# Kernel optimization log

Hardware: AMD Instinct MI355X
Metric: run time of the kernel (lower is better)

Reference implementation:

```python
import jax, jax.numpy as jnp
import numpy as np

C = 32            # multiplicity per irrep (node irreps = 32x0e + 32x1o)
N_NODES = 50000
N_EDGES = 800000
R_DIM = 8         # radial embedding dim
R_HID = 8         # radial MLP hidden width
N_SPECIES = 5
AVG_NEIGH = 16.0
N_PATHS = 4       # 0ex0e->0e, 0ex1o->1o, 1ox0e->1o, 1ox1o->0e


def setup_inputs() -> dict:
    key = jax.random.key(0)
    ks = jax.random.split(key, 16)
    inp = {
        'node_features': jax.random.normal(ks[0], (N_NODES, 4 * C), jnp.float32),
        'edge_features': jax.random.normal(ks[1], (N_EDGES, 4), jnp.float32),
        'radial_embedding': jax.random.normal(ks[2], (N_EDGES, R_DIM), jnp.float32),
        'senders': jax.random.randint(ks[3], (N_EDGES,), 0, N_NODES),
        'receivers': jax.random.randint(ks[4], (N_EDGES,), 0, N_NODES),
        'node_species': jax.random.randint(ks[5], (N_NODES,), 0, N_SPECIES),
        # linear_up: per-irrep (block-diagonal) mixing
        'W_up_s': jax.random.normal(ks[6], (C, C), jnp.float32),
        'W_up_v': jax.random.normal(ks[7], (C, C), jnp.float32),
        # radial MLP (no biases, e3nn-style): R_DIM -> R_HID -> N_PATHS*C
        'W_r1': jax.random.normal(ks[8], (R_DIM, R_HID), jnp.float32),
        'W_r2': jax.random.normal(ks[9], (R_HID, N_PATHS * C), jnp.float32),
        # linear_down: 2C x 0e -> 2C (C feats + C gates); 2C x 1o -> C x 1o
        'W_down_s': jax.random.normal(ks[10], (2 * C, 2 * C), jnp.float32),
        'W_down_v': jax.random.normal(ks[11], (2 * C, C), jnp.float32),
        # species-indexed skip connection to gate irreps
        'W_skip_s': jax.random.normal(ks[12], (N_SPECIES, C, 2 * C), jnp.float32),
        'W_skip_v': jax.random.normal(ks[13], (N_SPECIES, C, C), jnp.float32),
    }
    return inp


def reference(node_features, edge_features, radial_embedding, senders, receivers,
              node_species, W_up_s, W_up_v, W_r1, W_r2, W_down_s, W_down_v,
              W_skip_s, W_skip_v):
    N = node_features.shape[0]
    inv_sqrt_C = 1.0 / np.sqrt(C)
    # split irreps: scalars [N,C] and vectors [N,C,3]
    s = node_features[:, :C]
    v = node_features[:, C:].reshape(N, C, 3)
    # ---- linear_up (block-diagonal irreps Linear, fan-in normalized) ----
    s_up = (s @ W_up_s) * inv_sqrt_C
    v_up = jnp.einsum('ncx,cd->ndx', v, W_up_v) * inv_sqrt_C
    # ---- radial MLP -> per-edge tensor-product path weights ----
    h = jax.nn.silu((radial_embedding @ W_r1) * (1.0 / np.sqrt(R_DIM)))
    w = ((h @ W_r2) * (1.0 / np.sqrt(R_HID))).reshape(-1, N_PATHS, C)  # [E,4,C]
    # ---- tensor product messages over edges ----
    sh0 = edge_features[:, 0]      # [E]  l=0
    sh1 = edge_features[:, 1:4]    # [E,3] l=1
    se = s_up[senders]             # [E,C]
    ve = v_up[senders]             # [E,C,3]
    m0 = jnp.concatenate([
        w[:, 0] * se * sh0[:, None],                                      # 0e x 0e -> 0e
        w[:, 3] * jnp.einsum('ecx,ex->ec', ve, sh1) * (1.0 / np.sqrt(3.0))  # 1o x 1o -> 0e
    ], axis=1)                                                            # [E,2C]
    m1 = jnp.concatenate([
        w[:, 1, :, None] * se[:, :, None] * sh1[:, None, :],              # 0e x 1o -> 1o
        w[:, 2, :, None] * ve * sh0[:, None, None],                       # 1o x 0e -> 1o
    ], axis=1)                                                            # [E,2C,3]
    # ---- scatter aggregate to receivers, normalize by sqrt(avg neigh) ----
    inv_sqrt_deg = 1.0 / np.sqrt(AVG_NEIGH)
    agg0 = jax.ops.segment_sum(m0, receivers, num_segments=N) * inv_sqrt_deg
    agg1 = jax.ops.segment_sum(m1, receivers, num_segments=N) * inv_sqrt_deg
    # ---- linear_down to gate irreps (2C x 0e: C feats + C gates; C x 1o) ----
    inv_sqrt_2C = 1.0 / np.sqrt(2 * C)
    sc = (agg0 @ W_down_s) * inv_sqrt_2C                     # [N,2C]
    vc = jnp.einsum('ncx,cd->ndx', agg1, W_down_v) * inv_sqrt_2C  # [N,C,3]
    # ---- species-indexed skip connection ----
    skip_s = jnp.einsum('nc,ncd->nd', s, W_skip_s[node_species]) * inv_sqrt_C
    skip_v = jnp.einsum('ncx,ncd->ndx', v, W_skip_v[node_species]) * inv_sqrt_C
    sc = 0.5 * (sc + skip_s)
    vc = 0.5 * (vc + skip_v)
    # ---- gated nonlinearity: silu on scalars, silu(gates) * vectors ----
    feats = jax.nn.silu(sc[:, :C])
    gates = jax.nn.silu(sc[:, C:])
    vg = vc * gates[:, :, None]
    return jnp.concatenate([feats, vg.reshape(N, 3 * C)], axis=1)  # [N,4C]
```

## Files before the change

kernel.cpp:

```cpp
#include <hip/hip_runtime.h>
#include <stdint.h>

__device__ __forceinline__ float b2f(unsigned short u) {
    union { uint32_t i; float f; } v; v.i = ((uint32_t)u) << 16; return v.f;
}
__device__ __forceinline__ unsigned short f2b(float f) {
    union { float f; uint32_t i; } v; v.f = f;
    uint32_t i = v.i;
    uint32_t r = (i + 0x7fffu + ((i >> 16) & 1u)) >> 16;
    return (unsigned short)r;
}
__device__ __forceinline__ float silu_f(float x) { return x / (1.f + __expf(-x)); }

template<bool BF>
__device__ __forceinline__ float ldin(const void* p, size_t i) {
    if (BF) return b2f(((const unsigned short*)p)[i]);
    return ((const float*)p)[i];
}
template<bool BF>
__device__ __forceinline__ void ld4(const void* p, size_t i, float o[4]) {
    if (BF) {
        const ushort4 u = *(const ushort4*)((const unsigned short*)p + i);
        o[0] = b2f(u.x); o[1] = b2f(u.y); o[2] = b2f(u.z); o[3] = b2f(u.w);
    } else {
        const float4 f = *(const float4*)((const float*)p + i);
        o[0] = f.x; o[1] = f.y; o[2] = f.z; o[3] = f.w;
    }
}
template<bool BF>
__device__ __forceinline__ void stout(void* p, size_t i, float v) {
    if (BF) ((unsigned short*)p)[i] = f2b(v);
    else    ((float*)p)[i] = v;
}

#define INV_SQRT_C   0.17677669529663687f
#define INV_SQRT_8   0.3535533905932738f
#define INV_SQRT_3   0.5773502691896258f
#define INV_SQRT_DEG 0.25f
#define INV_SQRT_2C  0.125f

__device__ __forceinline__ bool detect_bf(const void* buf) {
    const int lane = threadIdx.x & 63;
    const uint32_t w = ((const uint32_t*)buf)[lane];
    const uint32_t ex = (w >> 7) & 0xFFu;
    const unsigned long long m = __ballot(ex >= 96u && ex <= 130u);
    return __popcll(m) > 32;
}

template<bool BF>
__device__ __forceinline__ void prep_nodes_body(
    const void* __restrict__ nf, const void* __restrict__ Wus,
    const void* __restrict__ Wuv, unsigned short* __restrict__ stage,
    int N, float* smem)
{
    float (*wsm)[128] = (float(*)[128])smem;
    const int wave = threadIdx.x >> 6;
    const int lane = threadIdx.x & 63;
    const int n = blockIdx.x * 4 + wave;
    if (n >= N) return;
    wsm[wave][lane]      = ldin<BF>(nf, (size_t)n * 128 + lane);
    wsm[wave][64 + lane] = ldin<BF>(nf, (size_t)n * 128 + 64 + lane);
    if (lane < 32) {
        float acc = 0.f;
        #pragma unroll 8
        for (int c = 0; c < 32; ++c) acc += wsm[wave][c] * ldin<BF>(Wus, c * 32 + lane);
        stage[(size_t)n * 128 + lane] = f2b(acc * INV_SQRT_C);
    } else {
        const int dd = lane - 32;
        float ax = 0.f, ay = 0.f, az = 0.f;
        #pragma unroll 8
        for (int c = 0; c < 32; ++c) {
            const float wv = ldin<BF>(Wuv, c * 32 + dd);
            ax += wsm[wave][32 + 3 * c    ] * wv;
            ay += wsm[wave][32 + 3 * c + 1] * wv;
            az += wsm[wave][32 + 3 * c + 2] * wv;
        }
        stage[(size_t)n * 128 + 32 + dd] = f2b(ax * INV_SQRT_C);
        stage[(size_t)n * 128 + 64 + dd] = f2b(ay * INV_SQRT_C);
        stage[(size_t)n * 128 + 96 + dd] = f2b(az * INV_SQRT_C);
    }
}
__global__ __launch_bounds__(256) void k_prep_nodes(
    const void* nf, const void* Wus, const void* Wuv,
    unsigned short* stage, int N)
{
    __shared__ float smem[4 * 128];
    if (detect_bf(nf)) prep_nodes_body<true >(nf, Wus, Wuv, stage, N, smem);
    else               prep_nodes_body<false>(nf, Wus, Wuv, stage, N, smem);
}

template<bool BF>
__device__ __forceinline__ void prep_edges_body(
    const void* __restrict__ radial, const int* __restrict__ senders,
    const int* __restrict__ recv, const void* __restrict__ Wr1,
    unsigned short* __restrict__ hbuf, int* __restrict__ counts,
    int* __restrict__ table, int* __restrict__ tableS,
    int* __restrict__ ovcnt, int* __restrict__ ovlist, int E)
{
    const int e = blockIdx.x * 256 + threadIdx.x;
    if (e >= E) return;
    const int rr  = recv[e];
    const int snd = senders[e];
    const int pos = atomicAdd(&counts[rr], 1);
    float r[8];
    ld4<BF>(radial, (size_t)e * 8, r);
    ld4<BF>(radial, (size_t)e * 8 + 4, r + 4);
    unsigned short h[8];
    #pragma unroll
    for (int j = 0; j < 8; ++j) {
        float pre = 0.f;
        #pragma unroll
        for (int k = 0; k < 8; ++k) pre += r[k] * ldin<BF>(Wr1, k * 8 + j);
        h[j] = f2b(silu_f(pre * INV_SQRT_8) * INV_SQRT_8);
    }
    ushort4* hp = (ushort4*)(hbuf + (size_t)e * 8);
    hp[0] = make_ushort4(h[0], h[1], h[2], h[3]);
    hp[1] = make_ushort4(h[4], h[5], h[6], h[7]);
    if (pos < 64) {
        table[(size_t)rr * 64 + pos] = e;
        if (tableS) tableS[(size_t)rr * 64 + pos] = snd;
    } else {
        ovlist[atomicAdd(ovcnt, 1)] = e;
    }
}
__global__ __launch_bounds__(256) void k_prep_edges(
    const void* radial, const int* senders, const int* recv, const void* Wr1,
    unsigned short* hbuf, int* counts, int* table, int* tableS,
    int* ovcnt, int* ovlist, int E)
{
    if (detect_bf(radial)) prep_edges_body<true >(radial, senders, recv, Wr1, hbuf,
                                                  counts, table, tableS, ovcnt, ovlist, E);
    else                   prep_edges_body<false>(radial, senders, recv, Wr1, hbuf,
                                                  counts, table, tableS, ovcnt, ovlist, E);
}

template<bool BF>
__device__ __forceinline__ void aggregate_body(
    const void* __restrict__ nf, const void* __restrict__ ef,
    const int* __restrict__ senders, const int* __restrict__ recv,
    const int* __restrict__ species,
    const void* __restrict__ Wr2, const void* __restrict__ Wds,
    const void* __restrict__ Wdv, const void* __restrict__ Wss,
    const void* __restrict__ Wsv,
    const unsigned short* __restrict__ stage,
    const unsigned short* __restrict__ hbuf,
    const int* __restrict__ counts, const int* __restrict__ table,
    const int* __restrict__ tableS,
    const int* __restrict__ ovcnt, const int* __restrict__ ovlist,
    void* __restrict__ out, int N, float* smem)
{
    float (*ldsM)[64][16] = (float(*)[64][16])smem;
    float (*ldsNF)[128]   = (float(*)[128])(smem + 4096);
    const int wave = threadIdx.x >> 6;
    const int lane = threadIdx.x & 63;
    const int n = blockIdx.x * 4 + wave;
    const bool valid = (n < N);
    const int d = lane - 32;
    int sp = 0, cnt = 0, mc = 0;
    float wA[8], wB[8];
    float acc0 = 0.f, a1x = 0.f, a1y = 0.f, a1z = 0.f;

    if (valid) {
        sp  = species[n];
        cnt = counts[n];
        mc  = (cnt < 64) ? cnt : 64;
        const int colA = (lane < 32) ? lane : lane + 32;
        #pragma unroll
        for (int j = 0; j < 8; ++j) {
            wA[j] = ldin<BF>(Wr2, j * 128 + colA);
            wB[j] = ldin<BF>(Wr2, j * 128 + colA + 32);
        }
        ldsNF[wave][lane]      = ldin<BF>(nf, (size_t)n * 128 + lane);
        ldsNF[wave][64 + lane] = ldin<BF>(nf, (size_t)n * 128 + 64 + lane);
        if (lane < mc) {
            const int eid = table[(size_t)n * 64 + lane];
            const int snd = tableS ? tableS[(size_t)n * 64 + lane]
                                   : senders[eid];
            float e4[4];
            if (BF) {
                const ushort4 u = *(const ushort4*)((const unsigned short*)ef + (size_t)eid * 4);
                e4[0] = b2f(u.x); e4[1] = b2f(u.y); e4[2] = b2f(u.z); e4[3] = b2f(u.w);
            } else {
                ld4<false>(ef, (size_t)eid * 4, e4);
            }
            const uint4 th = *(const uint4*)(hbuf + (size_t)eid * 8);
            float* M = ldsM[wave][lane];
            ((float4*)M)[0] = make_float4(e4[0], e4[1], e4[2], e4[3]);
            ((float4*)M)[1] = make_float4(b2f((unsigned short)(th.x & 0xFFFFu)),
                                          b2f((unsigned short)(th.x >> 16)),
                                          b2f((unsigned short)(th.y & 0xFFFFu)),
                                          b2f((unsigned short)(th.y >> 16)));
            ((float4*)M)[2] = make_float4(b2f((unsigned short)(th.z & 0xFFFFu)),
                                          b2f((unsigned short)(th.z >> 16)),
                                          b2f((unsigned short)(th.w & 0xFFFFu)),
                                          b2f((unsigned short)(th.w >> 16)));
            M[12] = __int_as_float(snd);
        }
    }

    if (valid && mc > 0) {
        auto gatherOne = [&](int idx, unsigned short& o0, unsigned short& o1,
                             unsigned short& o2) {
            const int snd = __float_as_int(ldsM[wave][idx][12]);
            const unsigned short* rec = stage + (size_t)snd * 128;
            if (lane < 32) { o0 = rec[lane]; }
            else { o0 = rec[32 + d]; o1 = rec[64 + d]; o2 = rec[96 + d]; }
        };
        auto edgeC = [&](int i, unsigned short s0, unsigned short s1,
                         unsigned short s2) {
            const float4 e4 = *((const float4*)&ldsM[wave][i][0]);
            const float4 ha = *((const float4*)&ldsM[wave][i][4]);
            const float4 hb = *((const float4*)&ldsM[wave][i][8]);
            const float vA = ha.x * wA[0] + ha.y * wA[1] + ha.z * wA[2] + ha.w * wA[3]
                           + hb.x * wA[4] + hb.y * wA[5] + hb.z * wA[6] + hb.w * wA[7];
            const float vB = ha.x * wB[0] + ha.y * wB[1] + ha.z * wB[2] + ha.w * wB[3]
                           + hb.x * wB[4] + hb.y * wB[5] + hb.z * wB[6] + hb.w * wB[7];
            if (lane < 32) {
                const float se = b2f(s0);
                acc0 += vA * se * e4.x;
                const float tt = vB * se;
                a1x += tt * e4.y; a1y += tt * e4.z; a1z += tt * e4.w;
            } else {
                const float vx = b2f(s0), vy = b2f(s1), vz = b2f(s2);
                acc0 += vB * (vx * e4.y + vy * e4.z + vz * e4.w);
                const float tt = vA * e4.x;
                a1x += tt * vx; a1y += tt * vy; a1z += tt * vz;
            }
        };
        unsigned short g0[8], g1[8], g2[8];
        int base = 0;
        for (; base + 8 <= mc; base += 8) {
            #pragma unroll
            for (int k = 0; k < 8; ++k) gatherOne(base + k, g0[k], g1[k], g2[k]);
            #pragma unroll
            for (int k = 0; k < 8; ++k) edgeC(base + k, g0[k], g1[k], g2[k]);
        }
        if (base < mc) {
            const int bc = mc - base;
            #pragma unroll
            for (int k = 0; k < 7; ++k) if (k < bc) gatherOne(base + k, g0[k], g1[k], g2[k]);
            #pragma unroll
            for (int k = 0; k < 7; ++k) if (k < bc) edgeC(base + k, g0[k], g1[k], g2[k]);
        }
    }
    if (valid && cnt > 64) {
        const int oc = *ovcnt;
        for (int i2 = 0; i2 < oc; ++i2) {
            const int e = ovlist[i2];
            if (recv[e] != n) continue;
            const int s = senders[e];
            float efv[4];
            ld4<BF>(ef, (size_t)e * 4, efv);
            const float sh0 = efv[0], s1x = efv[1], s1y = efv[2], s1z = efv[3];
            float h[8];
            #pragma unroll
            for (int j = 0; j < 8; ++j) h[j] = b2f(hbuf[(size_t)e * 8 + j]);
            const float vA = h[0] * wA[0] + h[1] * wA[1] + h[2] * wA[2] + h[3] * wA[3]
                           + h[4] * wA[4] + h[5] * wA[5] + h[6] * wA[6] + h[7] * wA[7];
            const float vB = h[0] * wB[0] + h[1] * wB[1] + h[2] * wB[2] + h[3] * wB[3]
                           + h[4] * wB[4] + h[5] * wB[5] + h[6] * wB[6] + h[7] * wB[7];
            const unsigned short* rec = stage + (size_t)s * 128;
            if (lane < 32) {
                const float se = b2f(rec[lane]);
                acc0 += vA * se * sh0;
                const float tt = vB * se;
                a1x += tt * s1x; a1y += tt * s1y; a1z += tt * s1z;
            } else {
                const float vx = b2f(rec[32 + d]), vy = b2f(rec[64 + d]), vz = b2f(rec[96 + d]);
                acc0 += vB * (vx * s1x + vy * s1y + vz * s1z);
                const float tt = vA * sh0;
                a1x += tt * vx; a1y += tt * vy; a1z += tt * vz;
            }
        }
    }
    if (valid && lane >= 32) acc0 *= INV_SQRT_3;

    __syncthreads();

    float* base_ = smem;
    float (*lds_agg0)[64]    = (float(*)[64])   base_;
    float (*lds_agg1)[3][65] = (float(*)[3][65])(base_ + 256);
    float (*lds_scf)[64]     = (float(*)[64])  (base_ + 1036);

    if (valid) {
        lds_agg0[wave][lane]    = acc0 * INV_SQRT_DEG;
        lds_agg1[wave][0][lane] = a1x * INV_SQRT_DEG;
        lds_agg1[wave][1][lane] = a1y * INV_SQRT_DEG;
        lds_agg1[wave][2][lane] = a1z * INV_SQRT_DEG;

        float sc = 0.f;
        #pragma unroll 8
        for (int c = 0; c < 64; ++c) sc += lds_agg0[wave][c] * ldin<BF>(Wds, c * 64 + lane);
        sc *= INV_SQRT_2C;
        float ss = 0.f;
        #pragma unroll 8
        for (int c = 0; c < 32; ++c)
            ss += ldsNF[wave][c] * ldin<BF>(Wss, (size_t)sp * 2048 + c * 64 + lane);
        ss *= INV_SQRT_C;
        lds_scf[wave][lane] = 0.5f * (sc + ss);

        #pragma unroll
        for (int rr = 0; rr < 2; ++rr) {
            const int p = lane + rr * 64;
            float outv;
            if (p < 32) {
                outv = silu_f(lds_scf[wave][p]);
            } else {
                const int o = p - 32;
                const int c = o / 3;
                const int x = o - 3 * c;
                float vc = 0.f;
                #pragma unroll 8
                for (int c2 = 0; c2 < 64; ++c2)
                    vc += lds_agg1[wave][x][c2] * ldin<BF>(Wdv, c2 * 32 + c);
                vc *= INV_SQRT_2C;
                float sv = 0.f;
                #pragma unroll 8
                for (int c2 = 0; c2 < 32; ++c2)
                    sv += ldsNF[wave][32 + c2 * 3 + x] * ldin<BF>(Wsv, (size_t)sp * 1024 + c2 * 32 + c);
                sv *= INV_SQRT_C;
                const float g = silu_f(lds_scf[wave][32 + c]);
                outv = 0.5f * (vc + sv) * g;
            }
            stout<BF>(out, (size_t)n * 128 + p, outv);
        }
    }
}
__global__ __launch_bounds__(256) void k_aggregate(
    const void* nf, const void* ef, const int* senders, const int* recv,
    const int* species,
    const void* Wr2, const void* Wds, const void* Wdv, const void* Wss, const void* Wsv,
    const unsigned short* stage, const unsigned short* hbuf,
    const int* counts, const int* table, const int* tableS,
    const int* ovcnt, const int* ovlist,
    void* out, int N)
{
    __shared__ float smem[4 * 64 * 16 + 4 * 128];
    if (detect_bf(nf)) aggregate_body<true >(nf, ef, senders, recv, species,
                                             Wr2, Wds, Wdv, Wss, Wsv,
                                             stage, hbuf, counts, table, tableS,
                                             ovcnt, ovlist, out, N, smem);
    else               aggregate_body<false>(nf, ef, senders, recv, species,
                                             Wr2, Wds, Wdv, Wss, Wsv,
                                             stage, hbuf, counts, table, tableS,
                                             ovcnt, ovlist, out, N, smem);
}

extern "C" void kernel_launch(void* const* d_in, const int* in_sizes, int n_in,
                              void* d_out, int out_size, void* d_ws, size_t ws_size,
                              hipStream_t stream) {
    const void* nf      = d_in[0];
    const void* ef      = d_in[1];
    const void* radial  = d_in[2];
    const int*  senders = (const int*)d_in[3];
    const int*  recv    = (const int*)d_in[4];
    const int*  specie  = (const int*)d_in[5];
    const void* Wus = d_in[6];
    const void* Wuv = d_in[7];
    const void* Wr1 = d_in[8];
    const void* Wr2 = d_in[9];
    const void* Wds = d_in[10];
    const void* Wdv = d_in[11];
    const void* Wss = d_in[12];
    const void* Wsv = d_in[13];

    const int N = in_sizes[5];
    const int E = in_sizes[3];

    const size_t stageB = (size_t)N * 128 * 2;
    const size_t hbufB  = (size_t)E * 8 * 2;
    const size_t tableB = (size_t)N * 64 * 4;
    const size_t miscB  = (size_t)(N + 1 + E) * 4;
    const size_t need1  = stageB + hbufB + tableB + miscB;
    const size_t need2  = need1 + tableB;
    if (ws_size < need1) return;

    char* ws = (char*)d_ws;
    unsigned short* stage = (unsigned short*)ws;
    unsigned short* hbuf  = (unsigned short*)(ws + stageB);
    int* table = (int*)(ws + stageB + hbufB);
    size_t off = stageB + hbufB + tableB;
    int* tableS = nullptr;
    if (ws_size >= need2) { tableS = (int*)(ws + off); off += tableB; }
    int* counts = (int*)(ws + off);
    int* ovcnt  = counts + N;
    int* ovlist = ovcnt + 1;

    hipMemsetAsync(counts, 0, (size_t)(N + 1) * sizeof(int), stream);

    k_prep_nodes<<<(N + 3) / 4, 256, 0, stream>>>(nf, Wus, Wuv, stage, N);
    k_prep_edges<<<(E + 255) / 256, 256, 0, stream>>>(radial, senders, recv, Wr1,
                                                      hbuf, counts, table, tableS,
                                                      ovcnt, ovlist, E);
    k_aggregate<<<(N + 3) / 4, 256, 0, stream>>>(nf, ef, senders, recv, specie,
                                                 Wr2, Wds, Wdv, Wss, Wsv,
                                                 stage, hbuf, counts, table, tableS,
                                                 ovcnt, ovlist, d_out, N);
}
```

Measured before the change: 470.2 us.

## Use persistent grid-stride prep kernels with register-cached weights and a branchless edge loop

The node and edge prep kernels become persistent grid-stride loops with fixed grid sizes. Each thread loads its weight column, or the whole 8x8 radial weight, into registers once instead of re-reading it per item. In the aggregate kernel, the per-edge sender gather uses precomputed byte offsets, and the lane-divergent scalar/vector branches are replaced by a select-based uniform computation. Risks are higher register pressure, with up to 64 extra floats per thread, and lower parallelism from the fixed grid sizes. The branchless form also does a few extra multiplies on the low lanes.

```diff
diff --git a/kernel.cpp b/kernel.cpp
--- a/kernel.cpp
+++ b/kernel.cpp
@@ -56,28 +56,33 @@
     float (*wsm)[128] = (float(*)[128])smem;
     const int wave = threadIdx.x >> 6;
     const int lane = threadIdx.x & 63;
-    const int n = blockIdx.x * 4 + wave;
-    if (n >= N) return;
-    wsm[wave][lane]      = ldin<BF>(nf, (size_t)n * 128 + lane);
-    wsm[wave][64 + lane] = ldin<BF>(nf, (size_t)n * 128 + 64 + lane);
-    if (lane < 32) {
-        float acc = 0.f;
-        #pragma unroll 8
-        for (int c = 0; c < 32; ++c) acc += wsm[wave][c] * ldin<BF>(Wus, c * 32 + lane);
-        stage[(size_t)n * 128 + lane] = f2b(acc * INV_SQRT_C);
-    } else {
-        const int dd = lane - 32;
-        float ax = 0.f, ay = 0.f, az = 0.f;
-        #pragma unroll 8
-        for (int c = 0; c < 32; ++c) {
-            const float wv = ldin<BF>(Wuv, c * 32 + dd);
-            ax += wsm[wave][32 + 3 * c    ] * wv;
-            ay += wsm[wave][32 + 3 * c + 1] * wv;
-            az += wsm[wave][32 + 3 * c + 2] * wv;
-        }
-        stage[(size_t)n * 128 + 32 + dd] = f2b(ax * INV_SQRT_C);
-        stage[(size_t)n * 128 + 64 + dd] = f2b(ay * INV_SQRT_C);
-        stage[(size_t)n * 128 + 96 + dd] = f2b(az * INV_SQRT_C);
+    const int dd = lane & 31;
+    const bool low = lane < 32;
+    float wcol[32];
+    #pragma unroll
+    for (int c = 0; c < 32; ++c)
+        wcol[c] = low ? ldin<BF>(Wus, c * 32 + dd) : ldin<BF>(Wuv, c * 32 + dd);
+    const int nw = gridDim.x * 4;
+    for (int n = blockIdx.x * 4 + wave; n < N; n += nw) {
+        wsm[wave][lane]      = ldin<BF>(nf, (size_t)n * 128 + lane);
+        wsm[wave][64 + lane] = ldin<BF>(nf, (size_t)n * 128 + 64 + lane);
+        if (low) {
+            float acc = 0.f;
+            #pragma unroll 8
+            for (int c = 0; c < 32; ++c) acc += wsm[wave][c] * wcol[c];
+            stage[(size_t)n * 128 + lane] = f2b(acc * INV_SQRT_C);
+        } else {
+            float ax = 0.f, ay = 0.f, az = 0.f;
+            #pragma unroll 8
+            for (int c = 0; c < 32; ++c) {
+                ax += wsm[wave][32 + 3 * c    ] * wcol[c];
+                ay += wsm[wave][32 + 3 * c + 1] * wcol[c];
+                az += wsm[wave][32 + 3 * c + 2] * wcol[c];
+            }
+            stage[(size_t)n * 128 + 32 + dd] = f2b(ax * INV_SQRT_C);
+            stage[(size_t)n * 128 + 64 + dd] = f2b(ay * INV_SQRT_C);
+            stage[(size_t)n * 128 + 96 + dd] = f2b(az * INV_SQRT_C);
+        }
     }
 }
 __global__ __launch_bounds__(256) void k_prep_nodes(
@@ -97,30 +102,35 @@
     int* __restrict__ table, int* __restrict__ tableS,
     int* __restrict__ ovcnt, int* __restrict__ ovlist, int E)
 {
-    const int e = blockIdx.x * 256 + threadIdx.x;
-    if (e >= E) return;
-    const int rr  = recv[e];
-    const int snd = senders[e];
-    const int pos = atomicAdd(&counts[rr], 1);
-    float r[8];
-    ld4<BF>(radial, (size_t)e * 8, r);
-    ld4<BF>(radial, (size_t)e * 8 + 4, r + 4);
-    unsigned short h[8];
+    float wr1[64];
     #pragma unroll
-    for (int j = 0; j < 8; ++j) {
-        float pre = 0.f;
+    for (int q = 0; q < 64; ++q) wr1[q] = ldin<BF>(Wr1, q);
+    const int stride = gridDim.x * 256;
+    #pragma unroll 2
+    for (int e = blockIdx.x * 256 + threadIdx.x; e < E; e += stride) {
+        const int rr  = recv[e];
+        const int snd = senders[e];
+        const int pos = atomicAdd(&counts[rr], 1);
+        float r[8];
+        ld4<BF>(radial, (size_t)e * 8, r);
+        ld4<BF>(radial, (size_t)e * 8 + 4, r + 4);
+        unsigned short h[8];
         #pragma unroll
-        for (int k = 0; k < 8; ++k) pre += r[k] * ldin<BF>(Wr1, k * 8 + j);
-        h[j] = f2b(silu_f(pre * INV_SQRT_8) * INV_SQRT_8);
-    }
-    ushort4* hp = (ushort4*)(hbuf + (size_t)e * 8);
-    hp[0] = make_ushort4(h[0], h[1], h[2], h[3]);
-    hp[1] = make_ushort4(h[4], h[5], h[6], h[7]);
-    if (pos < 64) {
-        table[(size_t)rr * 64 + pos] = e;
-        if (tableS) tableS[(size_t)rr * 64 + pos] = snd;
-    } else {
-        ovlist[atomicAdd(ovcnt, 1)] = e;
+        for (int j = 0; j < 8; ++j) {
+            float pre = 0.f;
+            #pragma unroll
+            for (int k = 0; k < 8; ++k) pre += r[k] * wr1[k * 8 + j];
+            h[j] = f2b(silu_f(pre * INV_SQRT_8) * INV_SQRT_8);
+        }
+        ushort4* hp = (ushort4*)(hbuf + (size_t)e * 8);
+        hp[0] = make_ushort4(h[0], h[1], h[2], h[3]);
+        hp[1] = make_ushort4(h[4], h[5], h[6], h[7]);
+        if (pos < 64) {
+            table[(size_t)rr * 64 + pos] = e;
+            if (tableS) tableS[(size_t)rr * 64 + pos] = snd;
+        } else {
+            ovlist[atomicAdd(ovcnt, 1)] = e;
+        }
     }
 }
 __global__ __launch_bounds__(256) void k_prep_edges(
@@ -155,16 +165,20 @@
     const int lane = threadIdx.x & 63;
     const int n = blockIdx.x * 4 + wave;
     const bool valid = (n < N);
-    const int d = lane - 32;
+    const bool low = lane < 32;
+    const int d = lane & 31;
     int sp = 0, cnt = 0, mc = 0;
     float wA[8], wB[8];
     float acc0 = 0.f, a1x = 0.f, a1y = 0.f, a1z = 0.f;
+    const uint32_t off0 = low ? (uint32_t)(lane << 1) : (uint32_t)(64 + (d << 1));
+    const uint32_t off1 = 128 + (d << 1);
+    const uint32_t off2 = 192 + (d << 1);
 
     if (valid) {
         sp  = species[n];
         cnt = counts[n];
         mc  = (cnt < 64) ? cnt : 64;
-        const int colA = (lane < 32) ? lane : lane + 32;
+        const int colA = low ? lane : lane + 32;
         #pragma unroll
         for (int j = 0; j < 8; ++j) {
             wA[j] = ldin<BF>(Wr2, j * 128 + colA);
@@ -202,12 +216,15 @@
         auto gatherOne = [&](int idx, unsigned short& o0, unsigned short& o1,
                              unsigned short& o2) {
             const int snd = __float_as_int(ldsM[wave][idx][12]);
-            const unsigned short* rec = stage + (size_t)snd * 128;
-            if (lane < 32) { o0 = rec[lane]; }
-            else { o0 = rec[32 + d]; o1 = rec[64 + d]; o2 = rec[96 + d]; }
+            const char* bp = (const char*)stage + (((uint32_t)snd) << 8);
+            o0 = *(const unsigned short*)(bp + off0);
+            if (!low) {
+                o1 = *(const unsigned short*)(bp + off1);
+                o2 = *(const unsigned short*)(bp + off2);
+            } else { o1 = 0; o2 = 0; }
         };
-        auto edgeC = [&](int i, unsigned short s0, unsigned short s1,
-                         unsigned short s2) {
+        auto edgeC = [&](int i, unsigned short s0u, unsigned short s1u,
+                         unsigned short s2u) {
             const float4 e4 = *((const float4*)&ldsM[wave][i][0]);
             const float4 ha = *((const float4*)&ldsM[wave][i][4]);
             const float4 hb = *((const float4*)&ldsM[wave][i][8]);
@@ -215,17 +232,18 @@
                            + hb.x * wA[4] + hb.y * wA[5] + hb.z * wA[6] + hb.w * wA[7];
             const float vB = ha.x * wB[0] + ha.y * wB[1] + ha.z * wB[2] + ha.w * wB[3]
                            + hb.x * wB[4] + hb.y * wB[5] + hb.z * wB[6] + hb.w * wB[7];
-            if (lane < 32) {
-                const float se = b2f(s0);
-                acc0 += vA * se * e4.x;
-                const float tt = vB * se;
-                a1x += tt * e4.y; a1y += tt * e4.z; a1z += tt * e4.w;
-            } else {
-                const float vx = b2f(s0), vy = b2f(s1), vz = b2f(s2);
-                acc0 += vB * (vx * e4.y + vy * e4.z + vz * e4.w);
-                const float tt = vA * e4.x;
-                a1x += tt * vx; a1y += tt * vy; a1z += tt * vz;
-            }
+            const float f0 = b2f(s0u), f1 = b2f(s1u), f2 = b2f(s2u);
+            const float wS = low ? vA   : vB;
+            const float wV = low ? vB   : vA;
+            const float G  = low ? f0   : e4.x;
+            const float m0 = low ? e4.x : e4.y;
+            const float Hx = low ? e4.y : f0;
+            const float Hy = low ? e4.z : f1;
+            const float Hz = low ? e4.w : f2;
+            const float dt = f0 * m0 + f1 * e4.z + f2 * e4.w;
+            acc0 += wS * dt;
+            const float t = wV * G;
+            a1x += t * Hx; a1y += t * Hy; a1z += t * Hz;
         };
         unsigned short g0[8], g1[8], g2[8];
         int base = 0;
@@ -260,7 +278,7 @@
             const float vB = h[0] * wB[0] + h[1] * wB[1] + h[2] * wB[2] + h[3] * wB[3]
                            + h[4] * wB[4] + h[5] * wB[5] + h[6] * wB[6] + h[7] * wB[7];
             const unsigned short* rec = stage + (size_t)s * 128;
-            if (lane < 32) {
+            if (low) {
                 const float se = b2f(rec[lane]);
                 acc0 += vA * se * sh0;
                 const float tt = vB * se;
@@ -273,7 +291,7 @@
             }
         }
     }
-    if (valid && lane >= 32) acc0 *= INV_SQRT_3;
+    if (valid && !low) acc0 *= INV_SQRT_3;
 
     __syncthreads();
 
@@ -388,10 +406,10 @@
 
     hipMemsetAsync(counts, 0, (size_t)(N + 1) * sizeof(int), stream);
 
-    k_prep_nodes<<<(N + 3) / 4, 256, 0, stream>>>(nf, Wus, Wuv, stage, N);
-    k_prep_edges<<<(E + 255) / 256, 256, 0, stream>>>(radial, senders, recv, Wr1,
-                                                      hbuf, counts, table, tableS,
-                                                      ovcnt, ovlist, E);
+    k_prep_nodes<<<2048, 256, 0, stream>>>(nf, Wus, Wuv, stage, N);
+    k_prep_edges<<<1024, 256, 0, stream>>>(radial, senders, recv, Wr1,
+                                           hbuf, counts, table, tableS,
+                                           ovcnt, ovlist, E);
     k_aggregate<<<(N + 3) / 4, 256, 0, stream>>>(nf, ef, senders, recv, specie,
                                                  Wr2, Wds, Wdv, Wss, Wsv,
                                                  stage, hbuf, counts, table, tableS,
```

Measured after the change: 543.6 us. +15.6%, slower.

## Pack per-edge data into 32-byte records and interleave staged node features

Applied to the files above, without the earlier changes.

The edge prep kernel now writes one 32-byte record per edge that holds the bf16 hidden radial features, the bf16 edge attributes and the sender id. This replaces the separate hbuf and tableS arrays plus the later edge_features read. Node staging is interleaved so each channel's scalar and xyz vector sit in 8 contiguous bytes, letting each aggregate lane fetch a sender's data with one 8-byte load. The aggregate kernel now handles 8 nodes per block with 32 lanes per node, each lane covering one channel for all four paths, and cooperatively preloads edge records into LDS. The trade-offs are more LDS per block, fewer lanes per node, and edge attributes rounded to bf16 in the fp32 path.

```diff
diff --git a/kernel.cpp b/kernel.cpp
--- a/kernel.cpp
+++ b/kernel.cpp
@@ -3,12 +3,21 @@
 
 __device__ __forceinline__ float b2f(unsigned short u) {
     union { uint32_t i; float f; } v; v.i = ((uint32_t)u) << 16; return v.f;
+}
+__device__ __forceinline__ float lo16(uint32_t u) {
+    union { uint32_t i; float f; } v; v.i = u << 16; return v.f;
+}
+__device__ __forceinline__ float hi16(uint32_t u) {
+    union { uint32_t i; float f; } v; v.i = u & 0xffff0000u; return v.f;
 }
 __device__ __forceinline__ unsigned short f2b(float f) {
     union { float f; uint32_t i; } v; v.f = f;
     uint32_t i = v.i;
     uint32_t r = (i + 0x7fffu + ((i >> 16) & 1u)) >> 16;
     return (unsigned short)r;
+}
+__device__ __forceinline__ uint32_t pk2(float a, float b) {
+    return (uint32_t)f2b(a) | ((uint32_t)f2b(b) << 16);
 }
 __device__ __forceinline__ float silu_f(float x) { return x / (1.f + __expf(-x)); }
 
@@ -51,22 +60,24 @@
 __device__ __forceinline__ void prep_nodes_body(
     const void* __restrict__ nf, const void* __restrict__ Wus,
     const void* __restrict__ Wuv, unsigned short* __restrict__ stage,
-    int N, float* smem)
-{
-    float (*wsm)[128] = (float(*)[128])smem;
+    int N, float* wsmf, unsigned short* outsu)
+{
+    float (*wsm)[128] = (float(*)[128])wsmf;
+    unsigned short (*outst)[128] = (unsigned short(*)[128])outsu;
     const int wave = threadIdx.x >> 6;
     const int lane = threadIdx.x & 63;
+    const int dd = lane & 31;
+    const bool low = lane < 32;
     const int n = blockIdx.x * 4 + wave;
     if (n >= N) return;
     wsm[wave][lane]      = ldin<BF>(nf, (size_t)n * 128 + lane);
     wsm[wave][64 + lane] = ldin<BF>(nf, (size_t)n * 128 + 64 + lane);
-    if (lane < 32) {
+    if (low) {
         float acc = 0.f;
         #pragma unroll 8
-        for (int c = 0; c < 32; ++c) acc += wsm[wave][c] * ldin<BF>(Wus, c * 32 + lane);
-        stage[(size_t)n * 128 + lane] = f2b(acc * INV_SQRT_C);
+        for (int c = 0; c < 32; ++c) acc += wsm[wave][c] * ldin<BF>(Wus, c * 32 + dd);
+        outst[wave][4 * dd] = f2b(acc * INV_SQRT_C);
     } else {
-        const int dd = lane - 32;
         float ax = 0.f, ay = 0.f, az = 0.f;
         #pragma unroll 8
         for (int c = 0; c < 32; ++c) {
@@ -75,27 +86,33 @@
             ay += wsm[wave][32 + 3 * c + 1] * wv;
             az += wsm[wave][32 + 3 * c + 2] * wv;
         }
-        stage[(size_t)n * 128 + 32 + dd] = f2b(ax * INV_SQRT_C);
-        stage[(size_t)n * 128 + 64 + dd] = f2b(ay * INV_SQRT_C);
-        stage[(size_t)n * 128 + 96 + dd] = f2b(az * INV_SQRT_C);
+        outst[wave][4 * dd + 1] = f2b(ax * INV_SQRT_C);
+        outst[wave][4 * dd + 2] = f2b(ay * INV_SQRT_C);
+        outst[wave][4 * dd + 3] = f2b(az * INV_SQRT_C);
+    }
+    if (low) {
+        *(uint2*)((char*)stage + (size_t)n * 256 + dd * 8) =
+            *(const uint2*)&outst[wave][4 * dd];
     }
 }
 __global__ __launch_bounds__(256) void k_prep_nodes(
     const void* nf, const void* Wus, const void* Wuv,
     unsigned short* stage, int N)
 {
-    __shared__ float smem[4 * 128];
-    if (detect_bf(nf)) prep_nodes_body<true >(nf, Wus, Wuv, stage, N, smem);
-    else               prep_nodes_body<false>(nf, Wus, Wuv, stage, N, smem);
+    __shared__ float wsmf[4 * 128];
+    __shared__ unsigned short outsu[4 * 128];
+    if (detect_bf(nf)) prep_nodes_body<true >(nf, Wus, Wuv, stage, N, wsmf, outsu);
+    else               prep_nodes_body<false>(nf, Wus, Wuv, stage, N, wsmf, outsu);
 }
 
 template<bool BF>
 __device__ __forceinline__ void prep_edges_body(
-    const void* __restrict__ radial, const int* __restrict__ senders,
-    const int* __restrict__ recv, const void* __restrict__ Wr1,
-    unsigned short* __restrict__ hbuf, int* __restrict__ counts,
-    int* __restrict__ table, int* __restrict__ tableS,
-    int* __restrict__ ovcnt, int* __restrict__ ovlist, int E)
+    const void* __restrict__ radial, const void* __restrict__ ef,
+    const int* __restrict__ senders, const int* __restrict__ recv,
+    const void* __restrict__ Wr1,
+    uint4* __restrict__ mtable, int* __restrict__ counts,
+    int* __restrict__ table, int* __restrict__ ovcnt,
+    int* __restrict__ ovlist, int E)
 {
     const int e = blockIdx.x * 256 + threadIdx.x;
     if (e >= E) return;
@@ -105,245 +122,260 @@
     float r[8];
     ld4<BF>(radial, (size_t)e * 8, r);
     ld4<BF>(radial, (size_t)e * 8 + 4, r + 4);
-    unsigned short h[8];
+    float h[8];
     #pragma unroll
     for (int j = 0; j < 8; ++j) {
         float pre = 0.f;
         #pragma unroll
         for (int k = 0; k < 8; ++k) pre += r[k] * ldin<BF>(Wr1, k * 8 + j);
-        h[j] = f2b(silu_f(pre * INV_SQRT_8) * INV_SQRT_8);
-    }
-    ushort4* hp = (ushort4*)(hbuf + (size_t)e * 8);
-    hp[0] = make_ushort4(h[0], h[1], h[2], h[3]);
-    hp[1] = make_ushort4(h[4], h[5], h[6], h[7]);
-    if (pos < 64) {
-        table[(size_t)rr * 64 + pos] = e;
-        if (tableS) tableS[(size_t)rr * 64 + pos] = snd;
+        h[j] = silu_f(pre * INV_SQRT_8) * INV_SQRT_8;
+    }
+    uint32_t e01, e23;
+    if (BF) {
+        const uint2 t = *(const uint2*)((const unsigned short*)ef + (size_t)e * 4);
+        e01 = t.x; e23 = t.y;
     } else {
-        ovlist[atomicAdd(ovcnt, 1)] = e;
-    }
+        const float4 f = *(const float4*)((const float*)ef + (size_t)e * 4);
+        e01 = pk2(f.x, f.y); e23 = pk2(f.z, f.w);
+    }
+    mtable[(size_t)e * 2    ] = make_uint4(pk2(h[0], h[1]), pk2(h[2], h[3]),
+                                           pk2(h[4], h[5]), pk2(h[6], h[7]));
+    mtable[(size_t)e * 2 + 1] = make_uint4(e01, e23, (uint32_t)snd, 0u);
+    if (pos < 64) table[(size_t)rr * 64 + pos] = e;
+    else          ovlist[atomicAdd(ovcnt, 1)] = e;
 }
 __global__ __launch_bounds__(256) void k_prep_edges(
-    const void* radial, const int* senders, const int* recv, const void* Wr1,
-    unsigned short* hbuf, int* counts, int* table, int* tableS,
+    const void* radial, const void* ef, const int* senders, const int* recv,
+    const void* Wr1, uint4* mtable, int* counts, int* table,
     int* ovcnt, int* ovlist, int E)
 {
-    if (detect_bf(radial)) prep_edges_body<true >(radial, senders, recv, Wr1, hbuf,
-                                                  counts, table, tableS, ovcnt, ovlist, E);
-    else                   prep_edges_body<false>(radial, senders, recv, Wr1, hbuf,
-                                                  counts, table, tableS, ovcnt, ovlist, E);
+    if (detect_bf(radial)) prep_edges_body<true >(radial, ef, senders, recv, Wr1,
+                                                  mtable, counts, table, ovcnt, ovlist, E);
+    else                   prep_edges_body<false>(radial, ef, senders, recv, Wr1,
+                                                  mtable, counts, table, ovcnt, ovlist, E);
 }
 
 template<bool BF>
 __device__ __forceinline__ void aggregate_body(
     const void* __restrict__ nf, const void* __restrict__ ef,
+    const void* __restrict__ radial,
     const int* __restrict__ senders, const int* __restrict__ recv,
     const int* __restrict__ species,
-    const void* __restrict__ Wr2, const void* __restrict__ Wds,
-    const void* __restrict__ Wdv, const void* __restrict__ Wss,
-    const void* __restrict__ Wsv,
+    const void* __restrict__ Wr1, const void* __restrict__ Wr2,
+    const void* __restrict__ Wds, const void* __restrict__ Wdv,
+    const void* __restrict__ Wss, const void* __restrict__ Wsv,
     const unsigned short* __restrict__ stage,
-    const unsigned short* __restrict__ hbuf,
+    const uint4* __restrict__ mt,
     const int* __restrict__ counts, const int* __restrict__ table,
-    const int* __restrict__ tableS,
     const int* __restrict__ ovcnt, const int* __restrict__ ovlist,
-    void* __restrict__ out, int N, float* smem)
-{
-    float (*ldsM)[64][16] = (float(*)[64][16])smem;
-    float (*ldsNF)[128]   = (float(*)[128])(smem + 4096);
-    const int wave = threadIdx.x >> 6;
-    const int lane = threadIdx.x & 63;
-    const int n = blockIdx.x * 4 + wave;
+    void* __restrict__ out, int N, uint32_t* smem)
+{
+    uint32_t (*ldsE)[64][8] = (uint32_t(*)[64][8])smem;
+    float (*ldsNF)[128] = (float(*)[128])(smem + 4096);
+    const int tid  = threadIdx.x;
+    const int wave = tid >> 6;
+    const int lane = tid & 63;
+    const int half = lane >> 5;
+    const int c    = lane & 31;
+    const int i    = wave * 2 + half;
+    const int bn   = blockIdx.x * 8;
+    const int n    = bn + i;
     const bool valid = (n < N);
-    const int d = lane - 32;
-    int sp = 0, cnt = 0, mc = 0;
-    float wA[8], wB[8];
-    float acc0 = 0.f, a1x = 0.f, a1y = 0.f, a1z = 0.f;
-
+
+    for (int idx = tid; idx < 512; idx += 256) {
+        const int ii = idx >> 6, j = idx & 63, ni = bn + ii;
+        if (ni < N) {
+            const int ct = counts[ni];
+            if (j < (ct < 64 ? ct : 64)) {
+                const int e = table[(size_t)ni * 64 + j];
+                const uint4 a = mt[(size_t)e * 2];
+                const uint4 b = mt[(size_t)e * 2 + 1];
+                *(uint4*)&ldsE[ii][j][0] = a;
+                *(uint4*)&ldsE[ii][j][4] = b;
+            }
+        }
+    }
+    for (int idx = tid; idx < 1024; idx += 256) {
+        const int ii = idx >> 7, f = idx & 127, ni = bn + ii;
+        if (ni < N) ldsNF[ii][f] = ldin<BF>(nf, (size_t)ni * 128 + f);
+    }
+    __syncthreads();
+
+    int cnt = 0, mc = 0;
+    float W0[8], W1[8], W2[8], W3[8];
+    float accS = 0.f, accD = 0.f;
+    float a1ax = 0.f, a1ay = 0.f, a1az = 0.f;
+    float a1bx = 0.f, a1by = 0.f, a1bz = 0.f;
     if (valid) {
-        sp  = species[n];
         cnt = counts[n];
         mc  = (cnt < 64) ? cnt : 64;
-        const int colA = (lane < 32) ? lane : lane + 32;
         #pragma unroll
         for (int j = 0; j < 8; ++j) {
-            wA[j] = ldin<BF>(Wr2, j * 128 + colA);
-            wB[j] = ldin<BF>(Wr2, j * 128 + colA + 32);
-        }
-        ldsNF[wave][lane]      = ldin<BF>(nf, (size_t)n * 128 + lane);
-        ldsNF[wave][64 + lane] = ldin<BF>(nf, (size_t)n * 128 + 64 + lane);
-        if (lane < mc) {
-            const int eid = table[(size_t)n * 64 + lane];
-            const int snd = tableS ? tableS[(size_t)n * 64 + lane]
-                                   : senders[eid];
-            float e4[4];
-            if (BF) {
-                const ushort4 u = *(const ushort4*)((const unsigned short*)ef + (size_t)eid * 4);
-                e4[0] = b2f(u.x); e4[1] = b2f(u.y); e4[2] = b2f(u.z); e4[3] = b2f(u.w);
-            } else {
-                ld4<false>(ef, (size_t)eid * 4, e4);
-            }
-            const uint4 th = *(const uint4*)(hbuf + (size_t)eid * 8);
-            float* M = ldsM[wave][lane];
-            ((float4*)M)[0] = make_float4(e4[0], e4[1], e4[2], e4[3]);
-            ((float4*)M)[1] = make_float4(b2f((unsigned short)(th.x & 0xFFFFu)),
-                                          b2f((unsigned short)(th.x >> 16)),
-                                          b2f((unsigned short)(th.y & 0xFFFFu)),
-                                          b2f((unsigned short)(th.y >> 16)));
-            ((float4*)M)[2] = make_float4(b2f((unsigned short)(th.z & 0xFFFFu)),
-                                          b2f((unsigned short)(th.z >> 16)),
-                                          b2f((unsigned short)(th.w & 0xFFFFu)),
-                                          b2f((unsigned short)(th.w >> 16)));
-            M[12] = __int_as_float(snd);
-        }
-    }
+            W0[j] = ldin<BF>(Wr2, (size_t)j * 128 + c);
+            W1[j] = ldin<BF>(Wr2, (size_t)j * 128 + 32 + c);
+            W2[j] = ldin<BF>(Wr2, (size_t)j * 128 + 64 + c);
+            W3[j] = ldin<BF>(Wr2, (size_t)j * 128 + 96 + c);
+        }
+    }
+    const char* stgb = (const char*)stage;
+    const uint32_t coff = (uint32_t)(c << 3);
+
+    auto EDGE = [&](int idx, uint2 pv) {
+        const uint4 A = *(const uint4*)&ldsE[i][idx][0];
+        const uint4 B = *(const uint4*)&ldsE[i][idx][4];
+        const float h0 = lo16(A.x), h1 = hi16(A.x), h2 = lo16(A.y), h3 = hi16(A.y);
+        const float h4 = lo16(A.z), h5 = hi16(A.z), h6 = lo16(A.w), h7 = hi16(A.w);
+        const float sh0 = lo16(B.x), s1x = hi16(B.x), s1y = lo16(B.y), s1z = hi16(B.y);
+        const float se = lo16(pv.x), vx = hi16(pv.x), vy = lo16(pv.y), vz = hi16(pv.y);
+        const float w0 = h0*W0[0]+h1*W0[1]+h2*W0[2]+h3*W0[3]+h4*W0[4]+h5*W0[5]+h6*W0[6]+h7*W0[7];
+        const float w1 = h0*W1[0]+h1*W1[1]+h2*W1[2]+h3*W1[3]+h4*W1[4]+h5*W1[5]+h6*W1[6]+h7*W1[7];
+        const float w2 = h0*W2[0]+h1*W2[1]+h2*W2[2]+h3*W2[3]+h4*W2[4]+h5*W2[5]+h6*W2[6]+h7*W2[7];
+        const float w3 = h0*W3[0]+h1*W3[1]+h2*W3[2]+h3*W3[3]+h4*W3[4]+h5*W3[5]+h6*W3[6]+h7*W3[7];
+        const float d3 = vx * s1x + vy * s1y + vz * s1z;
+        accS += w0 * (se * sh0);
+        accD += w3 * d3;
+        const float t1 = w1 * se;
+        a1ax += t1 * s1x; a1ay += t1 * s1y; a1az += t1 * s1z;
+        const float t2 = w2 * sh0;
+        a1bx += t2 * vx;  a1by += t2 * vy;  a1bz += t2 * vz;
+    };
 
     if (valid && mc > 0) {
-        auto gatherOne = [&](int idx, unsigned short& o0, unsigned short& o1,
-                             unsigned short& o2) {
-            const int snd = __float_as_int(ldsM[wave][idx][12]);
-            const unsigned short* rec = stage + (size_t)snd * 128;
-            if (lane < 32) { o0 = rec[lane]; }
-            else { o0 = rec[32 + d]; o1 = rec[64 + d]; o2 = rec[96 + d]; }
-        };
-        auto edgeC = [&](int i, unsigned short s0, unsigned short s1,
-                         unsigned short s2) {
-            const float4 e4 = *((const float4*)&ldsM[wave][i][0]);
-            const float4 ha = *((const float4*)&ldsM[wave][i][4]);
-            const float4 hb = *((const float4*)&ldsM[wave][i][8]);
-            const float vA = ha.x * wA[0] + ha.y * wA[1] + ha.z * wA[2] + ha.w * wA[3]
-                           + hb.x * wA[4] + hb.y * wA[5] + hb.z * wA[6] + hb.w * wA[7];
-            const float vB = ha.x * wB[0] + ha.y * wB[1] + ha.z * wB[2] + ha.w * wB[3]
-                           + hb.x * wB[4] + hb.y * wB[5] + hb.z * wB[6] + hb.w * wB[7];
-            if (lane < 32) {
-                const float se = b2f(s0);
-                acc0 += vA * se * e4.x;
-                const float tt = vB * se;
-                a1x += tt * e4.y; a1y += tt * e4.z; a1z += tt * e4.w;
-            } else {
-                const float vx = b2f(s0), vy = b2f(s1), vz = b2f(s2);
-                acc0 += vB * (vx * e4.y + vy * e4.z + vz * e4.w);
-                const float tt = vA * e4.x;
-                a1x += tt * vx; a1y += tt * vy; a1z += tt * vz;
-            }
-        };
-        unsigned short g0[8], g1[8], g2[8];
+        uint2 pf[8];
         int base = 0;
         for (; base + 8 <= mc; base += 8) {
             #pragma unroll
-            for (int k = 0; k < 8; ++k) gatherOne(base + k, g0[k], g1[k], g2[k]);
+            for (int k = 0; k < 8; ++k) {
+                const size_t snd = (size_t)ldsE[i][base + k][6];
+                pf[k] = *(const uint2*)(stgb + (snd << 8) + coff);
+            }
             #pragma unroll
-            for (int k = 0; k < 8; ++k) edgeC(base + k, g0[k], g1[k], g2[k]);
-        }
-        if (base < mc) {
-            const int bc = mc - base;
-            #pragma unroll
-            for (int k = 0; k < 7; ++k) if (k < bc) gatherOne(base + k, g0[k], g1[k], g2[k]);
-            #pragma unroll
-            for (int k = 0; k < 7; ++k) if (k < bc) edgeC(base + k, g0[k], g1[k], g2[k]);
-        }
+            for (int k = 0; k < 8; ++k) EDGE(base + k, pf[k]);
+        }
+        const int bc = mc - base;
+        #pragma unroll
+        for (int k = 0; k < 7; ++k) if (k < bc) {
+            const size_t snd = (size_t)ldsE[i][base + k][6];
+            pf[k] = *(const uint2*)(stgb + (snd << 8) + coff);
+        }
+        #pragma unroll
+        for (int k = 0; k < 7; ++k) if (k < bc) EDGE(base + k, pf[k]);
     }
     if (valid && cnt > 64) {
         const int oc = *ovcnt;
-        for (int i2 = 0; i2 < oc; ++i2) {
-            const int e = ovlist[i2];
+        for (int q = 0; q < oc; ++q) {
+            const int e = ovlist[q];
             if (recv[e] != n) continue;
-            const int s = senders[e];
-            float efv[4];
-            ld4<BF>(ef, (size_t)e * 4, efv);
-            const float sh0 = efv[0], s1x = efv[1], s1y = efv[2], s1z = efv[3];
-            float h[8];
+            const int snd = senders[e];
+            float ev[4];
+            ld4<BF>(ef, (size_t)e * 4, ev);
+            float r8[8];
+            ld4<BF>(radial, (size_t)e * 8, r8);
+            ld4<BF>(radial, (size_t)e * 8 + 4, r8 + 4);
+            float hh[8];
             #pragma unroll
-            for (int j = 0; j < 8; ++j) h[j] = b2f(hbuf[(size_t)e * 8 + j]);
-            const float vA = h[0] * wA[0] + h[1] * wA[1] + h[2] * wA[2] + h[3] * wA[3]
-                           + h[4] * wA[4] + h[5] * wA[5] + h[6] * wA[6] + h[7] * wA[7];
-            const float vB = h[0] * wB[0] + h[1] * wB[1] + h[2] * wB[2] + h[3] * wB[3]
-                           + h[4] * wB[4] + h[5] * wB[5] + h[6] * wB[6] + h[7] * wB[7];
-            const unsigned short* rec = stage + (size_t)s * 128;
-            if (lane < 32) {
-                const float se = b2f(rec[lane]);
-                acc0 += vA * se * sh0;
-                const float tt = vB * se;
-                a1x += tt * s1x; a1y += tt * s1y; a1z += tt * s1z;
-            } else {
-                const float vx = b2f(rec[32 + d]), vy = b2f(rec[64 + d]), vz = b2f(rec[96 + d]);
-                acc0 += vB * (vx * s1x + vy * s1y + vz * s1z);
-                const float tt = vA * sh0;
-                a1x += tt * vx; a1y += tt * vy; a1z += tt * vz;
+            for (int j = 0; j < 8; ++j) {
+                float pre = 0.f;
+                #pragma unroll
+                for (int k2 = 0; k2 < 8; ++k2) pre += r8[k2] * ldin<BF>(Wr1, k2 * 8 + j);
+                hh[j] = silu_f(pre * INV_SQRT_8) * INV_SQRT_8;
             }
-        }
-    }
-    if (valid && lane >= 32) acc0 *= INV_SQRT_3;
+            const uint2 pv = *(const uint2*)(stgb + ((size_t)(uint32_t)snd << 8) + coff);
+            const float se = lo16(pv.x), vx = hi16(pv.x), vy = lo16(pv.y), vz = hi16(pv.y);
+            const float w0 = hh[0]*W0[0]+hh[1]*W0[1]+hh[2]*W0[2]+hh[3]*W0[3]+hh[4]*W0[4]+hh[5]*W0[5]+hh[6]*W0[6]+hh[7]*W0[7];
+            const float w1 = hh[0]*W1[0]+hh[1]*W1[1]+hh[2]*W1[2]+hh[3]*W1[3]+hh[4]*W1[4]+hh[5]*W1[5]+hh[6]*W1[6]+hh[7]*W1[7];
+            const float w2 = hh[0]*W2[0]+hh[1]*W2[1]+hh[2]*W2[2]+hh[3]*W2[3]+hh[4]*W2[4]+hh[5]*W2[5]+hh[6]*W2[6]+hh[7]*W2[7];
+            const float w3 = hh[0]*W3[0]+hh[1]*W3[1]+hh[2]*W3[2]+hh[3]*W3[3]+hh[4]*W3[4]+hh[5]*W3[5]+hh[6]*W3[6]+hh[7]*W3[7];
+            const float d3 = vx * ev[1] + vy * ev[2] + vz * ev[3];
+            accS += w0 * (se * ev[0]);
+            accD += w3 * d3;
+            const float t1 = w1 * se;
+            a1ax += t1 * ev[1]; a1ay += t1 * ev[2]; a1az += t1 * ev[3];
+            const float t2 = w2 * ev[0];
+            a1bx += t2 * vx;  a1by += t2 * vy;  a1bz += t2 * vz;
+        }
+    }
+    if (valid) {
+        accS *= INV_SQRT_DEG;
+        accD *= INV_SQRT_DEG * INV_SQRT_3;
+        a1ax *= INV_SQRT_DEG; a1ay *= INV_SQRT_DEG; a1az *= INV_SQRT_DEG;
+        a1bx *= INV_SQRT_DEG; a1by *= INV_SQRT_DEG; a1bz *= INV_SQRT_DEG;
+    }
 
     __syncthreads();
 
-    float* base_ = smem;
-    float (*lds_agg0)[64]    = (float(*)[64])   base_;
-    float (*lds_agg1)[3][65] = (float(*)[3][65])(base_ + 256);
-    float (*lds_scf)[64]     = (float(*)[64])  (base_ + 1036);
+    float* bf_ = (float*)smem;
+    float (*agg0)[64]    = (float(*)[64])   bf_;
+    float (*agg1)[3][65] = (float(*)[3][65])(bf_ + 512);
+    float (*scf)[64]     = (float(*)[64])  (bf_ + 2072);
 
     if (valid) {
-        lds_agg0[wave][lane]    = acc0 * INV_SQRT_DEG;
-        lds_agg1[wave][0][lane] = a1x * INV_SQRT_DEG;
-        lds_agg1[wave][1][lane] = a1y * INV_SQRT_DEG;
-        lds_agg1[wave][2][lane] = a1z * INV_SQRT_DEG;
-
+        agg0[i][c]      = accS;
+        agg0[i][32 + c] = accD;
+        agg1[i][0][c] = a1ax; agg1[i][1][c] = a1ay; agg1[i][2][c] = a1az;
+        agg1[i][0][32 + c] = a1bx; agg1[i][1][32 + c] = a1by; agg1[i][2][32 + c] = a1bz;
+    }
+    #pragma unroll
+    for (int r = 0; r < 2; ++r) {
+        const int i2 = wave * 2 + r;
+        const int ni = bn + i2;
+        if (ni >= N) continue;
+        const int spn = species[ni];
         float sc = 0.f;
         #pragma unroll 8
-        for (int c = 0; c < 64; ++c) sc += lds_agg0[wave][c] * ldin<BF>(Wds, c * 64 + lane);
+        for (int c2 = 0; c2 < 64; ++c2) sc += agg0[i2][c2] * ldin<BF>(Wds, (size_t)c2 * 64 + lane);
         sc *= INV_SQRT_2C;
         float ss = 0.f;
         #pragma unroll 8
-        for (int c = 0; c < 32; ++c)
-            ss += ldsNF[wave][c] * ldin<BF>(Wss, (size_t)sp * 2048 + c * 64 + lane);
+        for (int c2 = 0; c2 < 32; ++c2)
+            ss += ldsNF[i2][c2] * ldin<BF>(Wss, (size_t)spn * 2048 + c2 * 64 + lane);
         ss *= INV_SQRT_C;
-        lds_scf[wave][lane] = 0.5f * (sc + ss);
-
+        scf[i2][lane] = 0.5f * (sc + ss);
         #pragma unroll
         for (int rr = 0; rr < 2; ++rr) {
             const int p = lane + rr * 64;
             float outv;
             if (p < 32) {
-                outv = silu_f(lds_scf[wave][p]);
+                outv = silu_f(scf[i2][p]);
             } else {
                 const int o = p - 32;
-                const int c = o / 3;
-                const int x = o - 3 * c;
+                const int cc = o / 3;
+                const int x = o - 3 * cc;
                 float vc = 0.f;
                 #pragma unroll 8
                 for (int c2 = 0; c2 < 64; ++c2)
-                    vc += lds_agg1[wave][x][c2] * ldin<BF>(Wdv, c2 * 32 + c);
+                    vc += agg1[i2][x][c2] * ldin<BF>(Wdv, (size_t)c2 * 32 + cc);
                 vc *= INV_SQRT_2C;
                 float sv = 0.f;
                 #pragma unroll 8
                 for (int c2 = 0; c2 < 32; ++c2)
-                    sv += ldsNF[wave][32 + c2 * 3 + x] * ldin<BF>(Wsv, (size_t)sp * 1024 + c2 * 32 + c);
+                    sv += ldsNF[i2][32 + c2 * 3 + x] * ldin<BF>(Wsv, (size_t)spn * 1024 + c2 * 32 + cc);
                 sv *= INV_SQRT_C;
-                const float g = silu_f(lds_scf[wave][32 + c]);
-                outv = 0.5f * (vc + sv) * g;
+                outv = 0.5f * (vc + sv) * silu_f(scf[i2][32 + cc]);
             }
-            stout<BF>(out, (size_t)n * 128 + p, outv);
+            stout<BF>(out, (size_t)ni * 128 + p, outv);
         }
     }
 }
 __global__ __launch_bounds__(256) void k_aggregate(
-    const void* nf, const void* ef, const int* senders, const int* recv,
-    const int* species,
-    const void* Wr2, const void* Wds, const void* Wdv, const void* Wss, const void* Wsv,
-    const unsigned short* stage, const unsigned short* hbuf,
-    const int* counts, const int* table, const int* tableS,
+    const void* nf, const void* ef, const void* radial,
+    const int* senders, const int* recv, const int* species,
+    const void* Wr1, const void* Wr2, const void* Wds, const void* Wdv,
+    const void* Wss, const void* Wsv,
+    const unsigned short* stage, const uint4* mt,
+    const int* counts, const int* table,
     const int* ovcnt, const int* ovlist,
     void* out, int N)
 {
-    __shared__ float smem[4 * 64 * 16 + 4 * 128];
-    if (detect_bf(nf)) aggregate_body<true >(nf, ef, senders, recv, species,
-                                             Wr2, Wds, Wdv, Wss, Wsv,
-                                             stage, hbuf, counts, table, tableS,
-                                             ovcnt, ovlist, out, N, smem);
-    else               aggregate_body<false>(nf, ef, senders, recv, species,
-                                             Wr2, Wds, Wdv, Wss, Wsv,
-                                             stage, hbuf, counts, table, tableS,
-                                             ovcnt, ovlist, out, N, smem);
+    __shared__ uint32_t smem[8 * 64 * 8 + 8 * 128];
+    if (detect_bf(nf)) aggregate_body<true >(nf, ef, radial, senders, recv, species,
+                                             Wr1, Wr2, Wds, Wdv, Wss, Wsv,
+                                             stage, mt, counts, table, ovcnt, ovlist,
+                                             out, N, smem);
+    else               aggregate_body<false>(nf, ef, radial, senders, recv, species,
+                                             Wr1, Wr2, Wds, Wdv, Wss, Wsv,
+                                             stage, mt, counts, table, ovcnt, ovlist,
+                                             out, N, smem);
 }
 
 extern "C" void kernel_launch(void* const* d_in, const int* in_sizes, int n_in,
@@ -368,32 +400,28 @@
     const int E = in_sizes[3];
 
     const size_t stageB = (size_t)N * 128 * 2;
-    const size_t hbufB  = (size_t)E * 8 * 2;
+    const size_t mtB    = (size_t)E * 32;
     const size_t tableB = (size_t)N * 64 * 4;
     const size_t miscB  = (size_t)(N + 1 + E) * 4;
-    const size_t need1  = stageB + hbufB + tableB + miscB;
-    const size_t need2  = need1 + tableB;
-    if (ws_size < need1) return;
+    const size_t need   = stageB + mtB + tableB + miscB;
+    if (ws_size < need) return;
 
     char* ws = (char*)d_ws;
     unsigned short* stage = (unsigned short*)ws;
-    unsigned short* hbuf  = (unsigned short*)(ws + stageB);
-    int* table = (int*)(ws + stageB + hbufB);
-    size_t off = stageB + hbufB + tableB;
-    int* tableS = nullptr;
-    if (ws_size >= need2) { tableS = (int*)(ws + off); off += tableB; }
-    int* counts = (int*)(ws + off);
-    int* ovcnt  = counts + N;
-    int* ovlist = ovcnt + 1;
+    uint4* mtable = (uint4*)(ws + stageB);
+    int* table    = (int*)(ws + stageB + mtB);
+    int* counts   = (int*)(ws + stageB + mtB + tableB);
+    int* ovcnt    = counts + N;
+    int* ovlist   = ovcnt + 1;
 
     hipMemsetAsync(counts, 0, (size_t)(N + 1) * sizeof(int), stream);
 
     k_prep_nodes<<<(N + 3) / 4, 256, 0, stream>>>(nf, Wus, Wuv, stage, N);
-    k_prep_edges<<<(E + 255) / 256, 256, 0, stream>>>(radial, senders, recv, Wr1,
-                                                      hbuf, counts, table, tableS,
+    k_prep_edges<<<(E + 255) / 256, 256, 0, stream>>>(radial, ef, senders, recv, Wr1,
+                                                      mtable, counts, table,
                                                       ovcnt, ovlist, E);
-    k_aggregate<<<(N + 3) / 4, 256, 0, stream>>>(nf, ef, senders, recv, specie,
-                                                 Wr2, Wds, Wdv, Wss, Wsv,
-                                                 stage, hbuf, counts, table, tableS,
+    k_aggregate<<<(N + 7) / 8, 256, 0, stream>>>(nf, ef, radial, senders, recv, specie,
+                                                 Wr1, Wr2, Wds, Wdv, Wss, Wsv,
+                                                 stage, mtable, counts, table,
                                                  ovcnt, ovlist, d_out, N);
 }
```

New measurement: 624.7 us. 32.9% more time.
